# Kernel tuning notes

Measured on AMD Instinct MI355X. Metric: run time of the kernel, lower is better.

The kernel has to match this reference:

```python
import jax, jax.numpy as jnp
import numpy as np

INPUT_DIM, LATENT_DIM, HIDDEN_DIM, BATCH = 1024, 128, 1024, 32768


def setup_inputs() -> dict:
    key = jax.random.key(0)
    ks = jax.random.split(key, 12)
    s = 0.02
    x = (jax.random.uniform(ks[0], (BATCH, INPUT_DIM)) < 0.5).astype(jnp.float32)  # binary data
    eps = jax.random.normal(ks[1], (BATCH, LATENT_DIM), dtype=jnp.float32)
    return {
        "x": x,
        "eps": eps,
        "We1": jax.random.normal(ks[2], (INPUT_DIM, HIDDEN_DIM)) * s,
        "be1": jnp.zeros((HIDDEN_DIM,), jnp.float32),
        "Wmu": jax.random.normal(ks[3], (HIDDEN_DIM, LATENT_DIM)) * s,
        "bmu": jnp.zeros((LATENT_DIM,), jnp.float32),
        "Wls": jax.random.normal(ks[4], (HIDDEN_DIM, LATENT_DIM)) * s,
        "bls": jnp.zeros((LATENT_DIM,), jnp.float32),
        "Wd1": jax.random.normal(ks[5], (LATENT_DIM, HIDDEN_DIM)) * s,
        "bd1": jnp.zeros((HIDDEN_DIM,), jnp.float32),
        "Wd2": jax.random.normal(ks[6], (HIDDEN_DIM, INPUT_DIM)) * s,
        "bd2": jnp.zeros((INPUT_DIM,), jnp.float32),
    }


def reference(x, eps, We1, be1, Wmu, bmu, Wls, bls, Wd1, bd1, Wd2, bd2):
    # Encoder: one hidden ReLU layer, mu / logsigma heads
    h = jax.nn.relu(x @ We1 + be1)                      # [B, H]
    mu = h @ Wmu + bmu                                  # [B, L]
    logsigma = h @ Wls + bls                            # [B, L]
    # Reparameterization: z = sigma * eps + mu (vectorized diag(exp(logsigma)) @ eps)
    z = mu + jnp.exp(logsigma) * eps                    # [B, L]
    # Decoder: one hidden ReLU layer, sigmoid Bernoulli params
    hd = jax.nn.relu(z @ Wd1 + bd1)                     # [B, H]
    theta = jax.nn.sigmoid(hd @ Wd2 + bd2)              # [B, D]
    # Bernoulli log-likelihood: sum_j log(theta^x * (1-theta)^(1-x))
    log_px = jnp.sum(x * jnp.log(theta) + (1.0 - x) * jnp.log1p(-theta), axis=-1)  # [B]
    # KL(q||N(0,I)) = 0.5 * sum(sigma^2 + mu^2 - log(sigma^2) - 1)
    kl = 0.5 * jnp.sum(jnp.exp(2.0 * logsigma) + mu * mu - 2.0 * logsigma - 1.0, axis=-1)  # [B]
    return log_px - kl                                  # elbo_mc [B]
```

## Files before the change

### kernel.cpp

```cpp
#include <hip/hip_runtime.h>
#include <cstdint>
#include <cstddef>


typedef __bf16 bf16x8 __attribute__((ext_vector_type(8)));
typedef float f32x4 __attribute__((ext_vector_type(4)));

__device__ __forceinline__ unsigned short f32_to_bf16(float f) {
  unsigned int u = __float_as_uint(f);
  u += 0x7fffu + ((u >> 16) & 1u);
  return (unsigned short)(u >> 16);
}

struct TransJob { const float* in; unsigned short* out; int K, N, blkEnd; };

__global__ void prep_k(TransJob j0, TransJob j1, TransJob j2,
                       TransJob j3, TransJob j4,
                       const float* __restrict__ x,
                       unsigned short* __restrict__ xbit,
                       int n4, int castBlocks) {
  __shared__ float tile[32][33];
  int bid = blockIdx.x;
  int tx = threadIdx.x, ty = threadIdx.y;
  if (bid >= j4.blkEnd) {
    int tid = ty * 32 + tx;
    int stride = castBlocks * 256;
    for (int i = (bid - j4.blkEnd) * 256 + tid; i < n4; i += stride) {
      float4 v = reinterpret_cast<const float4*>(x)[i];
      unsigned int nib = (v.x != 0.f ? 1u : 0u) | (v.y != 0.f ? 2u : 0u) |
                         (v.z != 0.f ? 4u : 0u) | (v.w != 0.f ? 8u : 0u);
      unsigned int n1 = __shfl_down(nib, 1, 64);
      unsigned int n2 = __shfl_down(nib, 2, 64);
      unsigned int n3 = __shfl_down(nib, 3, 64);
      if ((tid & 3) == 0)
        xbit[i >> 2] = (unsigned short)(nib | (n1 << 4) | (n2 << 8) | (n3 << 12));
    }
    return;
  }
  TransJob j; int base;
  if (bid < j0.blkEnd)      { j = j0; base = 0; }
  else if (bid < j1.blkEnd) { j = j1; base = j0.blkEnd; }
  else if (bid < j2.blkEnd) { j = j2; base = j1.blkEnd; }
  else if (bid < j3.blkEnd) { j = j3; base = j2.blkEnd; }
  else                      { j = j4; base = j3.blkEnd; }
  int local = bid - base;
  int gxN = j.N >> 5;
  int n0 = (local % gxN) * 32, k0 = (local / gxN) * 32;
#pragma unroll
  for (int r = 0; r < 32; r += 8)
    tile[ty + r][tx] = j.in[(size_t)(k0 + ty + r) * j.N + n0 + tx];
  __syncthreads();
#pragma unroll
  for (int r = 0; r < 32; r += 8)
    j.out[(size_t)(n0 + ty + r) * j.K + k0 + tx] = f32_to_bf16(tile[tx][ty + r]);
}

__device__ __forceinline__ void gl_lds16(const unsigned short* g, unsigned short* l) {
  __builtin_amdgcn_global_load_lds(
      (__attribute__((address_space(1))) void*)g,
      (__attribute__((address_space(3))) void*)l, 16, 0, 0);
}

template <int EPI, int TAG, int ABIT>
__global__ __launch_bounds__(512, 2) void gemm256(
    const unsigned short* __restrict__ A, const unsigned short* __restrict__ BT,
    int gx, int N, int K,
    const float* __restrict__ bias0,
    unsigned short* __restrict__ outb, float* __restrict__ outf,
    const unsigned short* __restrict__ xbit) {
  __shared__ __align__(16) unsigned short smem[65536];

  const int tid = threadIdx.x;
  const int lane = tid & 63;
  const int wave = tid >> 6;
  const int wr = wave >> 2;
  const int wc = wave & 3;
  const int lm = lane & 15, lq = lane >> 4;
  const int sw = lm & 7;

  const int bid = blockIdx.x;
  const int xcd = bid & 7;
  const int t8 = bid >> 3;
  const int m0 = (xcd + 8 * (t8 / gx)) * 256;
  const int n0 = (t8 % gx) * 256;
  const int NT = K >> 6;

  unsigned short* const smemp = smem;
  auto Abuf = [&](int b) -> unsigned short* {
    return ABIT ? smemp : smemp + b * 32768;
  };
  auto Bbuf = [&](int b) -> unsigned short* {
    return ABIT ? smemp + 16384 + b * 16384 : smemp + b * 32768 + 16384;
  };

  const unsigned short* gpA[2];
  const unsigned short* gpB[2];
  int loA[2], loB[2], xaddr[2];
#pragma unroll
  for (int r = 0; r < 2; ++r) {
    int c = tid + 512 * r, rl = c >> 3, q8 = c & 7;
    int rowA = (rl & 63) + ((rl >> 6) << 7);
    int rowB = (rl & 31) + ((rl >> 5) << 6);
    int qgA = q8 ^ (rowA & 7);
    gpA[r] = A + (size_t)(m0 + rowA) * K + qgA * 8;
    gpB[r] = BT + (size_t)(n0 + rowB) * K + (q8 ^ (rowB & 7)) * 8;
    loA[r] = rowA * 64 + q8 * 8;
    loB[r] = rowB * 64 + q8 * 8;
    xaddr[r] = rowA * 128 + qgA;
  }

  auto stage = [&](int kind, int buf, int kt) {
#pragma unroll
    for (int r = 0; r < 2; ++r) {
      if (kind == 0)      { if (!ABIT) gl_lds16(gpA[r] + kt * 64,          Abuf(buf) + loA[r]); }
      else if (kind == 3) { if (!ABIT) gl_lds16(gpA[r] + 64 * K + kt * 64, Abuf(buf) + loA[r] + 4096); }
      else if (kind == 1) gl_lds16(gpB[r] + kt * 64,          Bbuf(buf) + loB[r]);
      else                gl_lds16(gpB[r] + 32 * K + kt * 64, Bbuf(buf) + loB[r] + 2048);
    }
  };

  auto expandA = [&](int t) {
    const unsigned char* xsb = reinterpret_cast<const unsigned char*>(smemp + 49152);
    unsigned short* As = smemp;
#pragma unroll
    for (int r = 0; r < 2; ++r) {
#pragma unroll
      for (int h = 0; h < 2; ++h) {
        unsigned int b = xsb[xaddr[r] + h * 8192 + 8 * t];
        unsigned int o0 = ((b & 1u)        ? 0x3F80u : 0u) | ((b & 2u)   ? 0x3F800000u : 0u);
        unsigned int o1 = (((b >> 2) & 1u) ? 0x3F80u : 0u) | ((b & 8u)   ? 0x3F800000u : 0u);
        unsigned int o2 = (((b >> 4) & 1u) ? 0x3F80u : 0u) | ((b & 32u)  ? 0x3F800000u : 0u);
        unsigned int o3 = (((b >> 6) & 1u) ? 0x3F80u : 0u) | ((b & 128u) ? 0x3F800000u : 0u);
        *reinterpret_cast<uint4*>(As + loA[r] + h * 4096) = make_uint4(o0, o1, o2, o3);
      }
    }
  };

  if (ABIT) {
    const unsigned short* xp = xbit + (size_t)m0 * 64;
    unsigned short* xs = smemp + 49152;
#pragma unroll
    for (int i = 0; i < 4; ++i)
      gl_lds16(xp + (tid + 512 * i) * 8, xs + (tid + 512 * i) * 8);
    stage(1, 0, 0); stage(2, 0, 0);
    stage(1, 1, 1); stage(2, 1, 1);
    asm volatile("s_waitcnt vmcnt(8)" ::: "memory");
    expandA(0);
    asm volatile("s_waitcnt vmcnt(4) lgkmcnt(0)" ::: "memory");
    __builtin_amdgcn_s_barrier();
  } else {
    stage(0, 0, 0); stage(1, 0, 0); stage(2, 0, 0); stage(3, 0, 0);
    stage(0, 1, 1); stage(1, 1, 1); stage(2, 1, 1);
    asm volatile("s_waitcnt vmcnt(6)" ::: "memory");
    __builtin_amdgcn_s_barrier();
  }

  f32x4 acc[8][4] = {};

  const int aRow = (wr * 128 + lm) * 64;
  const int bRow = (wc * 64 + lm) * 64;
  const int c0 = ((0 | lq) ^ sw) * 8;
  const int c1 = ((4 | lq) ^ sw) * 8;

  for (int t = 0; t < NT; ++t) {
    const int b = t & 1;
    const unsigned short* Ab = Abuf(b);
    const unsigned short* Bb = Bbuf(b);
    bf16x8 af[4][2], bf1[2][2], bf2[2][2];

#pragma unroll
    for (int i = 0; i < 4; ++i) {
      af[i][0] = *reinterpret_cast<const bf16x8*>(Ab + aRow + i * 1024 + c0);
      af[i][1] = *reinterpret_cast<const bf16x8*>(Ab + aRow + i * 1024 + c1);
    }
#pragma unroll
    for (int j = 0; j < 2; ++j) {
      bf1[j][0] = *reinterpret_cast<const bf16x8*>(Bb + bRow + j * 1024 + c0);
      bf1[j][1] = *reinterpret_cast<const bf16x8*>(Bb + bRow + j * 1024 + c1);
    }
    if (!ABIT && t + 1 < NT) stage(3, (t + 1) & 1, t + 1);
    __builtin_amdgcn_s_barrier();
    asm volatile("s_waitcnt lgkmcnt(0)" ::: "memory");
    __builtin_amdgcn_sched_barrier(0);
    __builtin_amdgcn_s_setprio(1);
#pragma unroll
    for (int s = 0; s < 2; ++s)
#pragma unroll
      for (int i = 0; i < 4; ++i)
#pragma unroll
        for (int j = 0; j < 2; ++j)
          acc[i][j] = __builtin_amdgcn_mfma_f32_16x16x32_bf16(af[i][s], bf1[j][s], acc[i][j], 0, 0, 0);
    __builtin_amdgcn_s_setprio(0);
    __builtin_amdgcn_s_barrier();

#pragma unroll
    for (int j = 0; j < 2; ++j) {
      bf2[j][0] = *reinterpret_cast<const bf16x8*>(Bb + bRow + (j + 2) * 1024 + c0);
      bf2[j][1] = *reinterpret_cast<const bf16x8*>(Bb + bRow + (j + 2) * 1024 + c1);
    }
    if (t + 2 < NT) stage(ABIT ? 1 : 0, b, t + 2);
    __builtin_amdgcn_s_barrier();
    asm volatile("s_waitcnt lgkmcnt(0)" ::: "memory");
    __builtin_amdgcn_sched_barrier(0);
    __builtin_amdgcn_s_setprio(1);
#pragma unroll
    for (int s = 0; s < 2; ++s)
#pragma unroll
      for (int i = 0; i < 4; ++i)
#pragma unroll
        for (int j = 0; j < 2; ++j)
          acc[i][j + 2] = __builtin_amdgcn_mfma_f32_16x16x32_bf16(af[i][s], bf2[j][s], acc[i][j + 2], 0, 0, 0);
    __builtin_amdgcn_s_setprio(0);
    __builtin_amdgcn_s_barrier();

#pragma unroll
    for (int i = 0; i < 4; ++i) {
      af[i][0] = *reinterpret_cast<const bf16x8*>(Ab + aRow + (64 + i * 16) * 64 + c0);
      af[i][1] = *reinterpret_cast<const bf16x8*>(Ab + aRow + (64 + i * 16) * 64 + c1);
    }
    if (t + 2 < NT) stage(ABIT ? 2 : 1, b, t + 2);
    __builtin_amdgcn_s_barrier();
    asm volatile("s_waitcnt lgkmcnt(0)" ::: "memory");
    __builtin_amdgcn_sched_barrier(0);
    __builtin_amdgcn_s_setprio(1);
#pragma unroll
    for (int s = 0; s < 2; ++s)
#pragma unroll
      for (int i = 0; i < 4; ++i)
#pragma unroll
        for (int j = 0; j < 2; ++j)
          acc[i + 4][j] = __builtin_amdgcn_mfma_f32_16x16x32_bf16(af[i][s], bf1[j][s], acc[i + 4][j], 0, 0, 0);
    __builtin_amdgcn_s_setprio(0);
    __builtin_amdgcn_s_barrier();

    if (ABIT) { if (t + 1 < NT) expandA(t + 1); }
    else      { if (t + 2 < NT) stage(2, b, t + 2); }
    __builtin_amdgcn_s_barrier();
    __builtin_amdgcn_s_setprio(1);
#pragma unroll
    for (int s = 0; s < 2; ++s)
#pragma unroll
      for (int i = 0; i < 4; ++i)
#pragma unroll
        for (int j = 0; j < 2; ++j)
          acc[i + 4][j + 2] = __builtin_amdgcn_mfma_f32_16x16x32_bf16(af[i][s], bf2[j][s], acc[i + 4][j + 2], 0, 0, 0);
    __builtin_amdgcn_s_setprio(0);
    if (ABIT) {
      if (t + 2 < NT) { asm volatile("s_waitcnt vmcnt(4) lgkmcnt(0)" ::: "memory"); }
      else            { asm volatile("s_waitcnt vmcnt(0) lgkmcnt(0)" ::: "memory"); }
    } else {
      if (t + 2 < NT)      { asm volatile("s_waitcnt vmcnt(6)" ::: "memory"); }
      else if (t + 1 < NT) { asm volatile("s_waitcnt vmcnt(0)" ::: "memory"); }
    }
    __builtin_amdgcn_s_barrier();
  }

  if (EPI == 0) {
#pragma unroll
    for (int i = 0; i < 8; ++i)
#pragma unroll
      for (int j = 0; j < 4; ++j) {
        int col = n0 + wc * 64 + j * 16 + lm;
        float bias = bias0[col];
#pragma unroll
        for (int r = 0; r < 4; ++r) {
          int row = m0 + wr * 128 + i * 16 + lq * 4 + r;
          float v = acc[i][j][r] + bias;
          outb[(size_t)row * N + col] = f32_to_bf16(fmaxf(v, 0.f));
        }
      }
  } else {
    const int wpr = N >> 4;
#pragma unroll
    for (int i = 0; i < 8; ++i) {
      float rs[4] = {0.f, 0.f, 0.f, 0.f};
#pragma unroll
      for (int j = 0; j < 4; ++j) {
        int col = n0 + wc * 64 + j * 16 + lm;
        float bias = bias0[col];
        int w16 = (col >> 4);
#pragma unroll
        for (int r = 0; r < 4; ++r) {
          int row = m0 + wr * 128 + i * 16 + lq * 4 + r;
          float l = acc[i][j][r] + bias;
          unsigned short mask = xbit[(size_t)row * wpr + w16];
          float tt = ((mask >> lm) & 1) ? -l : l;
          float sp = fmaxf(tt, 0.f) + __logf(1.f + __expf(-fabsf(tt)));
          rs[r] -= sp;
        }
      }
#pragma unroll
      for (int off = 1; off < 16; off <<= 1)
#pragma unroll
        for (int r = 0; r < 4; ++r) rs[r] += __shfl_xor(rs[r], off, 64);
      if (lm == 0) {
#pragma unroll
        for (int r = 0; r < 4; ++r)
          atomicAdd(&outf[m0 + wr * 128 + i * 16 + lq * 4 + r], rs[r]);
      }
    }
  }
}

__global__ __launch_bounds__(256, 2) void latent_fused(
    const unsigned short* A,
    const unsigned short* __restrict__ BT,
    const unsigned short* __restrict__ WD1,
    const float* __restrict__ bmu, const float* __restrict__ bls,
    const float* __restrict__ bd1,
    const float* __restrict__ eps,
    unsigned short* hd,
    float* __restrict__ out) {
  __shared__ __align__(16) unsigned short smem[28672];
  unsigned short* As0 = smem;
  unsigned short* As1 = smem + 2048;
  unsigned short* Bs0 = smem + 4096;
  unsigned short* Bs1 = smem + 12288;
  unsigned short* zs  = smem + 20480;
  unsigned short* Bs2 = smem;

  const int K = 1024;
  const int tid = threadIdx.x;
  const int lane = tid & 63;
  const int wave = tid >> 6;
  const int m0 = blockIdx.x * 64;
  const int lm = lane & 15, lq = lane >> 4;
  const int sw2 = (lm >> 1) & 3;

  const unsigned short* agp;
  const unsigned short* bgp[4];
  {
    int row = tid >> 2, q = tid & 3;
    agp = A + (size_t)(m0 + row) * K + (q ^ ((row >> 1) & 3)) * 8;
  }
#pragma unroll
  for (int r = 0; r < 4; ++r) {
    int c = tid + 256 * r;
    int row = c >> 2, q = c & 3;
    bgp[r] = BT + (size_t)row * K + (q ^ ((row >> 1) & 3)) * 8;
  }

  auto stage1 = [&](int buf, int kt) {
    gl_lds16(agp + kt, (buf ? As1 : As0) + tid * 8);
    unsigned short* Bd = buf ? Bs1 : Bs0;
#pragma unroll
    for (int r = 0; r < 4; ++r) gl_lds16(bgp[r] + kt, Bd + (tid + 256 * r) * 8);
  };

  f32x4 acc[16] = {};

  stage1(0, 0);
  __syncthreads();

  const int aOff = (wave * 16 + lm) * 32 + (lq ^ sw2) * 8;
  for (int t = 0; t < 32; ++t) {
    const int cur = t & 1;
    if (t + 1 < 32) stage1(cur ^ 1, (t + 1) * 32);
    const unsigned short* Ab = cur ? As1 : As0;
    const unsigned short* Bb = cur ? Bs1 : Bs0;
    bf16x8 af = *reinterpret_cast<const bf16x8*>(Ab + aOff);
#pragma unroll
    for (int j = 0; j < 16; ++j) {
      bf16x8 b = *reinterpret_cast<const bf16x8*>(Bb + (j * 16 + lm) * 32 + (lq ^ sw2) * 8);
      acc[j] = __builtin_amdgcn_mfma_f32_16x16x32_bf16(af, b, acc[j], 0, 0, 0);
    }
    __syncthreads();
  }

  auto stage2 = [&](int hh) {
#pragma unroll
    for (int ri = 0; ri < 8; ++ri) {
      int c = tid + 256 * ri;
      int row = c >> 4, slot = c & 15;
      int gc = slot ^ (row & 7);
      gl_lds16(WD1 + (size_t)(hh * 128 + row) * 128 + gc * 8, Bs2 + c * 8);
    }
  };
  stage2(0);

  {
    float kl[4] = {0.f, 0.f, 0.f, 0.f};
#pragma unroll
    for (int j = 0; j < 8; ++j) {
      int dim = j * 16 + lm;
      float bm = bmu[dim], bl = bls[dim];
#pragma unroll
      for (int r = 0; r < 4; ++r) {
        int rowl = wave * 16 + lq * 4 + r;
        float mu = acc[j][r] + bm;
        float ls = acc[j + 8][r] + bl;
        float e = eps[(size_t)(m0 + rowl) * 128 + dim];
        float zv = fmaf(__expf(ls), e, mu);
        int chunk = (dim >> 3);
        int slot = chunk ^ (rowl & 7);
        zs[rowl * 128 + slot * 8 + (lm & 7)] = f32_to_bf16(zv);
        kl[r] += 0.5f * (__expf(2.f * ls) + mu * mu - 2.f * ls - 1.f);
      }
    }
#pragma unroll
    for (int off = 1; off < 16; off <<= 1)
#pragma unroll
      for (int r = 0; r < 4; ++r) kl[r] += __shfl_xor(kl[r], off, 64);
    if (lm == 0) {
#pragma unroll
      for (int r = 0; r < 4; ++r)
        out[m0 + wave * 16 + lq * 4 + r] = -kl[r];
    }
  }

  for (int hh = 0; hh < 8; ++hh) {
    asm volatile("s_waitcnt vmcnt(0)" ::: "memory");
    __syncthreads();
    f32x4 acc2[8] = {};
#pragma unroll
    for (int ks = 0; ks < 4; ++ks) {
      const int cks = (ks * 4 + lq) ^ (lm & 7);
      bf16x8 a0 = *reinterpret_cast<const bf16x8*>(zs + (wave * 16 + lm) * 128 + cks * 8);
#pragma unroll
      for (int j = 0; j < 8; ++j) {
        bf16x8 b = *reinterpret_cast<const bf16x8*>(Bs2 + (j * 16 + lm) * 128 + cks * 8);
        acc2[j] = __builtin_amdgcn_mfma_f32_16x16x32_bf16(a0, b, acc2[j], 0, 0, 0);
      }
    }
    __syncthreads();
    if (hh + 1 < 8) stage2(hh + 1);
#pragma unroll
    for (int j = 0; j < 8; ++j) {
      int col = hh * 128 + j * 16 + lm;
      float bias = bd1[col];
#pragma unroll
      for (int r = 0; r < 4; ++r) {
        int row = m0 + wave * 16 + lq * 4 + r;
        float v = acc2[j][r] + bias;
        hd[(size_t)row * 1024 + col] = f32_to_bf16(fmaxf(v, 0.f));
      }
    }
  }
}

extern "C" void kernel_launch(void* const* d_in, const int* in_sizes, int n_in,
                              void* d_out, int out_size, void* d_ws, size_t ws_size,
                              hipStream_t stream) {
  const float* x   = (const float*)d_in[0];
  const float* eps = (const float*)d_in[1];
  const float* We1 = (const float*)d_in[2];
  const float* be1 = (const float*)d_in[3];
  const float* Wmu = (const float*)d_in[4];
  const float* bmu = (const float*)d_in[5];
  const float* Wls = (const float*)d_in[6];
  const float* bls = (const float*)d_in[7];
  const float* Wd1 = (const float*)d_in[8];
  const float* bd1 = (const float*)d_in[9];
  const float* Wd2 = (const float*)d_in[10];
  const float* bd2 = (const float*)d_in[11];
  float* out = (float*)d_out;

  const int B = 32768, D = 1024, H = 1024, L = 128;

  char* ws = (char*)d_ws;
  size_t off = 0;
  auto alloc = [&](size_t bytes) {
    void* p = ws + off;
    off += (bytes + 255) & ~(size_t)255;
    return p;
  };
  unsigned short* xbit = (unsigned short*)alloc((size_t)B * D / 8);
  unsigned short* w1t  = (unsigned short*)alloc((size_t)H * D * 2);
  unsigned short* w2t  = (unsigned short*)alloc((size_t)256 * H * 2);
  unsigned short* wd1t = (unsigned short*)alloc((size_t)H * L * 2);
  unsigned short* wd2t = (unsigned short*)alloc((size_t)D * H * 2);
  unsigned short* h    = (unsigned short*)alloc((size_t)B * H * 2);
  unsigned short* hd   = h;

  TransJob j0{We1, w1t, D, H, 1024};
  TransJob j1{Wmu, w2t, H, L, 1152};
  TransJob j2{Wls, w2t + 128 * H, H, L, 1280};
  TransJob j3{Wd1, wd1t, L, H, 1408};
  TransJob j4{Wd2, wd2t, H, D, 2432};
  prep_k<<<2432 + 2048, dim3(32, 8), 0, stream>>>(
      j0, j1, j2, j3, j4, x, xbit, B * D / 4, 2048);

  gemm256<0, 1, 1><<<512, 512, 0, stream>>>(
      nullptr, w1t, 4, H, D, be1, h, nullptr, xbit);
  latent_fused<<<B / 64, 256, 0, stream>>>(
      h, w2t, wd1t, bmu, bls, bd1, eps, hd, out);
  gemm256<2, 4, 0><<<512, 512, 0, stream>>>(
      hd, wd2t, 4, D, H, bd2, nullptr, out, xbit);

  (void)in_sizes; (void)n_in; (void)out_size; (void)ws_size;
}
```

Baseline: 430.2 us.

## Loop two N tiles per block in first GEMM, split decoder GEMM, double-buffer Wd1

The first GEMM now launches 256 blocks, and each block loops over two 256-column N tiles, reusing the bit-packed x row block already loaded into LDS. The decoder output GEMM is split into two launches covering the two halves of the M dimension. The latent kernel's Wd1 staging becomes double-buffered 64-row chunks, so the next chunk is prefetched while the current one computes instead of sitting behind a full sync. The goal is to cut redundant x loads and hide weight-load latency, at the cost of fewer blocks per launch and one extra kernel launch.

```diff
diff --git a/kernel.cpp b/kernel.cpp
--- a/kernel.cpp
+++ b/kernel.cpp
@@ -64,7 +64,7 @@
 template <int EPI, int TAG, int ABIT>
 __global__ __launch_bounds__(512, 2) void gemm256(
     const unsigned short* __restrict__ A, const unsigned short* __restrict__ BT,
-    int gx, int N, int K,
+    int mBase, int N, int K,
     const float* __restrict__ bias0,
     unsigned short* __restrict__ outb, float* __restrict__ outf,
     const unsigned short* __restrict__ xbit) {
@@ -81,8 +81,9 @@
   const int bid = blockIdx.x;
   const int xcd = bid & 7;
   const int t8 = bid >> 3;
-  const int m0 = (xcd + 8 * (t8 / gx)) * 256;
-  const int n0 = (t8 % gx) * 256;
+  int m0, n0base;
+  if (ABIT) { m0 = (xcd + 8 * (t8 >> 1)) * 256; n0base = (t8 & 1) * 512; }
+  else      { m0 = mBase + (xcd + 8 * (t8 >> 2)) * 256; n0base = (t8 & 3) * 256; }
   const int NT = K >> 6;
 
   unsigned short* const smemp = smem;
@@ -94,7 +95,7 @@
   };
 
   const unsigned short* gpA[2];
-  const unsigned short* gpB[2];
+  const unsigned short* gpB0[2];
   int loA[2], loB[2], xaddr[2];
 #pragma unroll
   for (int r = 0; r < 2; ++r) {
@@ -103,21 +104,11 @@
     int rowB = (rl & 31) + ((rl >> 5) << 6);
     int qgA = q8 ^ (rowA & 7);
     gpA[r] = A + (size_t)(m0 + rowA) * K + qgA * 8;
-    gpB[r] = BT + (size_t)(n0 + rowB) * K + (q8 ^ (rowB & 7)) * 8;
+    gpB0[r] = BT + (size_t)rowB * K + (q8 ^ (rowB & 7)) * 8;
     loA[r] = rowA * 64 + q8 * 8;
     loB[r] = rowB * 64 + q8 * 8;
     xaddr[r] = rowA * 128 + qgA;
   }
-
-  auto stage = [&](int kind, int buf, int kt) {
-#pragma unroll
-    for (int r = 0; r < 2; ++r) {
-      if (kind == 0)      { if (!ABIT) gl_lds16(gpA[r] + kt * 64,          Abuf(buf) + loA[r]); }
-      else if (kind == 3) { if (!ABIT) gl_lds16(gpA[r] + 64 * K + kt * 64, Abuf(buf) + loA[r] + 4096); }
-      else if (kind == 1) gl_lds16(gpB[r] + kt * 64,          Bbuf(buf) + loB[r]);
-      else                gl_lds16(gpB[r] + 32 * K + kt * 64, Bbuf(buf) + loB[r] + 2048);
-    }
-  };
 
   auto expandA = [&](int t) {
     const unsigned char* xsb = reinterpret_cast<const unsigned char*>(smemp + 49152);
@@ -136,167 +127,187 @@
     }
   };
 
-  if (ABIT) {
-    const unsigned short* xp = xbit + (size_t)m0 * 64;
-    unsigned short* xs = smemp + 49152;
-#pragma unroll
-    for (int i = 0; i < 4; ++i)
-      gl_lds16(xp + (tid + 512 * i) * 8, xs + (tid + 512 * i) * 8);
-    stage(1, 0, 0); stage(2, 0, 0);
-    stage(1, 1, 1); stage(2, 1, 1);
-    asm volatile("s_waitcnt vmcnt(8)" ::: "memory");
-    expandA(0);
-    asm volatile("s_waitcnt vmcnt(4) lgkmcnt(0)" ::: "memory");
-    __builtin_amdgcn_s_barrier();
-  } else {
-    stage(0, 0, 0); stage(1, 0, 0); stage(2, 0, 0); stage(3, 0, 0);
-    stage(0, 1, 1); stage(1, 1, 1); stage(2, 1, 1);
-    asm volatile("s_waitcnt vmcnt(6)" ::: "memory");
-    __builtin_amdgcn_s_barrier();
-  }
-
-  f32x4 acc[8][4] = {};
-
   const int aRow = (wr * 128 + lm) * 64;
   const int bRow = (wc * 64 + lm) * 64;
   const int c0 = ((0 | lq) ^ sw) * 8;
   const int c1 = ((4 | lq) ^ sw) * 8;
 
-  for (int t = 0; t < NT; ++t) {
-    const int b = t & 1;
-    const unsigned short* Ab = Abuf(b);
-    const unsigned short* Bb = Bbuf(b);
-    bf16x8 af[4][2], bf1[2][2], bf2[2][2];
-
-#pragma unroll
-    for (int i = 0; i < 4; ++i) {
-      af[i][0] = *reinterpret_cast<const bf16x8*>(Ab + aRow + i * 1024 + c0);
-      af[i][1] = *reinterpret_cast<const bf16x8*>(Ab + aRow + i * 1024 + c1);
-    }
-#pragma unroll
-    for (int j = 0; j < 2; ++j) {
-      bf1[j][0] = *reinterpret_cast<const bf16x8*>(Bb + bRow + j * 1024 + c0);
-      bf1[j][1] = *reinterpret_cast<const bf16x8*>(Bb + bRow + j * 1024 + c1);
-    }
-    if (!ABIT && t + 1 < NT) stage(3, (t + 1) & 1, t + 1);
-    __builtin_amdgcn_s_barrier();
-    asm volatile("s_waitcnt lgkmcnt(0)" ::: "memory");
-    __builtin_amdgcn_sched_barrier(0);
-    __builtin_amdgcn_s_setprio(1);
-#pragma unroll
-    for (int s = 0; s < 2; ++s)
-#pragma unroll
-      for (int i = 0; i < 4; ++i)
-#pragma unroll
-        for (int j = 0; j < 2; ++j)
-          acc[i][j] = __builtin_amdgcn_mfma_f32_16x16x32_bf16(af[i][s], bf1[j][s], acc[i][j], 0, 0, 0);
-    __builtin_amdgcn_s_setprio(0);
-    __builtin_amdgcn_s_barrier();
-
-#pragma unroll
-    for (int j = 0; j < 2; ++j) {
-      bf2[j][0] = *reinterpret_cast<const bf16x8*>(Bb + bRow + (j + 2) * 1024 + c0);
-      bf2[j][1] = *reinterpret_cast<const bf16x8*>(Bb + bRow + (j + 2) * 1024 + c1);
-    }
-    if (t + 2 < NT) stage(ABIT ? 1 : 0, b, t + 2);
-    __builtin_amdgcn_s_barrier();
-    asm volatile("s_waitcnt lgkmcnt(0)" ::: "memory");
-    __builtin_amdgcn_sched_barrier(0);
-    __builtin_amdgcn_s_setprio(1);
-#pragma unroll
-    for (int s = 0; s < 2; ++s)
-#pragma unroll
-      for (int i = 0; i < 4; ++i)
-#pragma unroll
-        for (int j = 0; j < 2; ++j)
-          acc[i][j + 2] = __builtin_amdgcn_mfma_f32_16x16x32_bf16(af[i][s], bf2[j][s], acc[i][j + 2], 0, 0, 0);
-    __builtin_amdgcn_s_setprio(0);
-    __builtin_amdgcn_s_barrier();
-
-#pragma unroll
-    for (int i = 0; i < 4; ++i) {
-      af[i][0] = *reinterpret_cast<const bf16x8*>(Ab + aRow + (64 + i * 16) * 64 + c0);
-      af[i][1] = *reinterpret_cast<const bf16x8*>(Ab + aRow + (64 + i * 16) * 64 + c1);
-    }
-    if (t + 2 < NT) stage(ABIT ? 2 : 1, b, t + 2);
-    __builtin_amdgcn_s_barrier();
-    asm volatile("s_waitcnt lgkmcnt(0)" ::: "memory");
-    __builtin_amdgcn_sched_barrier(0);
-    __builtin_amdgcn_s_setprio(1);
-#pragma unroll
-    for (int s = 0; s < 2; ++s)
-#pragma unroll
-      for (int i = 0; i < 4; ++i)
-#pragma unroll
-        for (int j = 0; j < 2; ++j)
-          acc[i + 4][j] = __builtin_amdgcn_mfma_f32_16x16x32_bf16(af[i][s], bf1[j][s], acc[i + 4][j], 0, 0, 0);
-    __builtin_amdgcn_s_setprio(0);
-    __builtin_amdgcn_s_barrier();
-
-    if (ABIT) { if (t + 1 < NT) expandA(t + 1); }
-    else      { if (t + 2 < NT) stage(2, b, t + 2); }
-    __builtin_amdgcn_s_barrier();
-    __builtin_amdgcn_s_setprio(1);
-#pragma unroll
-    for (int s = 0; s < 2; ++s)
-#pragma unroll
-      for (int i = 0; i < 4; ++i)
-#pragma unroll
-        for (int j = 0; j < 2; ++j)
-          acc[i + 4][j + 2] = __builtin_amdgcn_mfma_f32_16x16x32_bf16(af[i][s], bf2[j][s], acc[i + 4][j + 2], 0, 0, 0);
-    __builtin_amdgcn_s_setprio(0);
+  const int NTL = ABIT ? 2 : 1;
+  for (int ntl = 0; ntl < NTL; ++ntl) {
+    const int n0 = n0base + ntl * 256;
+    const unsigned short* gB[2];
+#pragma unroll
+    for (int r = 0; r < 2; ++r) gB[r] = gpB0[r] + (size_t)n0 * K;
+
+    auto stage = [&](int kind, int buf, int kt) {
+#pragma unroll
+      for (int r = 0; r < 2; ++r) {
+        if (kind == 0)      { if (!ABIT) gl_lds16(gpA[r] + kt * 64,          Abuf(buf) + loA[r]); }
+        else if (kind == 3) { if (!ABIT) gl_lds16(gpA[r] + 64 * K + kt * 64, Abuf(buf) + loA[r] + 4096); }
+        else if (kind == 1) gl_lds16(gB[r] + kt * 64,          Bbuf(buf) + loB[r]);
+        else                gl_lds16(gB[r] + 32 * K + kt * 64, Bbuf(buf) + loB[r] + 2048);
+      }
+    };
+
     if (ABIT) {
-      if (t + 2 < NT) { asm volatile("s_waitcnt vmcnt(4) lgkmcnt(0)" ::: "memory"); }
-      else            { asm volatile("s_waitcnt vmcnt(0) lgkmcnt(0)" ::: "memory"); }
+      if (ntl == 0) {
+        const unsigned short* xp = xbit + (size_t)m0 * 64;
+        unsigned short* xs = smemp + 49152;
+#pragma unroll
+        for (int i = 0; i < 4; ++i)
+          gl_lds16(xp + (tid + 512 * i) * 8, xs + (tid + 512 * i) * 8);
+      }
+      stage(1, 0, 0); stage(2, 0, 0);
+      stage(1, 1, 1); stage(2, 1, 1);
+      if (ntl == 0) { asm volatile("s_waitcnt vmcnt(8)" ::: "memory"); }
+      expandA(0);
+      asm volatile("s_waitcnt vmcnt(4) lgkmcnt(0)" ::: "memory");
+      __builtin_amdgcn_s_barrier();
     } else {
-      if (t + 2 < NT)      { asm volatile("s_waitcnt vmcnt(6)" ::: "memory"); }
-      else if (t + 1 < NT) { asm volatile("s_waitcnt vmcnt(0)" ::: "memory"); }
-    }
-    __builtin_amdgcn_s_barrier();
-  }
-
-  if (EPI == 0) {
-#pragma unroll
-    for (int i = 0; i < 8; ++i)
-#pragma unroll
-      for (int j = 0; j < 4; ++j) {
-        int col = n0 + wc * 64 + j * 16 + lm;
-        float bias = bias0[col];
-#pragma unroll
-        for (int r = 0; r < 4; ++r) {
-          int row = m0 + wr * 128 + i * 16 + lq * 4 + r;
-          float v = acc[i][j][r] + bias;
-          outb[(size_t)row * N + col] = f32_to_bf16(fmaxf(v, 0.f));
+      stage(0, 0, 0); stage(1, 0, 0); stage(2, 0, 0); stage(3, 0, 0);
+      stage(0, 1, 1); stage(1, 1, 1); stage(2, 1, 1);
+      asm volatile("s_waitcnt vmcnt(6)" ::: "memory");
+      __builtin_amdgcn_s_barrier();
+    }
+
+    f32x4 acc[8][4] = {};
+
+    for (int t = 0; t < NT; ++t) {
+      const int b = t & 1;
+      const unsigned short* Ab = Abuf(b);
+      const unsigned short* Bb = Bbuf(b);
+      bf16x8 af[4][2], bf1[2][2], bf2[2][2];
+
+#pragma unroll
+      for (int i = 0; i < 4; ++i) {
+        af[i][0] = *reinterpret_cast<const bf16x8*>(Ab + aRow + i * 1024 + c0);
+        af[i][1] = *reinterpret_cast<const bf16x8*>(Ab + aRow + i * 1024 + c1);
+      }
+#pragma unroll
+      for (int j = 0; j < 2; ++j) {
+        bf1[j][0] = *reinterpret_cast<const bf16x8*>(Bb + bRow + j * 1024 + c0);
+        bf1[j][1] = *reinterpret_cast<const bf16x8*>(Bb + bRow + j * 1024 + c1);
+      }
+      if (!ABIT && t + 1 < NT) stage(3, (t + 1) & 1, t + 1);
+      __builtin_amdgcn_s_barrier();
+      asm volatile("s_waitcnt lgkmcnt(0)" ::: "memory");
+      __builtin_amdgcn_sched_barrier(0);
+      __builtin_amdgcn_s_setprio(1);
+#pragma unroll
+      for (int s = 0; s < 2; ++s)
+#pragma unroll
+        for (int i = 0; i < 4; ++i)
+#pragma unroll
+          for (int j = 0; j < 2; ++j)
+            acc[i][j] = __builtin_amdgcn_mfma_f32_16x16x32_bf16(af[i][s], bf1[j][s], acc[i][j], 0, 0, 0);
+      __builtin_amdgcn_s_setprio(0);
+      __builtin_amdgcn_s_barrier();
+
+#pragma unroll
+      for (int j = 0; j < 2; ++j) {
+        bf2[j][0] = *reinterpret_cast<const bf16x8*>(Bb + bRow + (j + 2) * 1024 + c0);
+        bf2[j][1] = *reinterpret_cast<const bf16x8*>(Bb + bRow + (j + 2) * 1024 + c1);
+      }
+      if (t + 2 < NT) stage(ABIT ? 1 : 0, b, t + 2);
+      __builtin_amdgcn_s_barrier();
+      asm volatile("s_waitcnt lgkmcnt(0)" ::: "memory");
+      __builtin_amdgcn_sched_barrier(0);
+      __builtin_amdgcn_s_setprio(1);
+#pragma unroll
+      for (int s = 0; s < 2; ++s)
+#pragma unroll
+        for (int i = 0; i < 4; ++i)
+#pragma unroll
+          for (int j = 0; j < 2; ++j)
+            acc[i][j + 2] = __builtin_amdgcn_mfma_f32_16x16x32_bf16(af[i][s], bf2[j][s], acc[i][j + 2], 0, 0, 0);
+      __builtin_amdgcn_s_setprio(0);
+      __builtin_amdgcn_s_barrier();
+
+#pragma unroll
+      for (int i = 0; i < 4; ++i) {
+        af[i][0] = *reinterpret_cast<const bf16x8*>(Ab + aRow + (64 + i * 16) * 64 + c0);
+        af[i][1] = *reinterpret_cast<const bf16x8*>(Ab + aRow + (64 + i * 16) * 64 + c1);
+      }
+      if (t + 2 < NT) stage(ABIT ? 2 : 1, b, t + 2);
+      __builtin_amdgcn_s_barrier();
+      asm volatile("s_waitcnt lgkmcnt(0)" ::: "memory");
+      __builtin_amdgcn_sched_barrier(0);
+      __builtin_amdgcn_s_setprio(1);
+#pragma unroll
+      for (int s = 0; s < 2; ++s)
+#pragma unroll
+        for (int i = 0; i < 4; ++i)
+#pragma unroll
+          for (int j = 0; j < 2; ++j)
+            acc[i + 4][j] = __builtin_amdgcn_mfma_f32_16x16x32_bf16(af[i][s], bf1[j][s], acc[i + 4][j], 0, 0, 0);
+      __builtin_amdgcn_s_setprio(0);
+      __builtin_amdgcn_s_barrier();
+
+      if (ABIT) { if (t + 1 < NT) expandA(t + 1); }
+      else      { if (t + 2 < NT) stage(2, b, t + 2); }
+      __builtin_amdgcn_s_barrier();
+      __builtin_amdgcn_s_setprio(1);
+#pragma unroll
+      for (int s = 0; s < 2; ++s)
+#pragma unroll
+        for (int i = 0; i < 4; ++i)
+#pragma unroll
+          for (int j = 0; j < 2; ++j)
+            acc[i + 4][j + 2] = __builtin_amdgcn_mfma_f32_16x16x32_bf16(af[i][s], bf2[j][s], acc[i + 4][j + 2], 0, 0, 0);
+      __builtin_amdgcn_s_setprio(0);
+      if (ABIT) {
+        if (t + 2 < NT) { asm volatile("s_waitcnt vmcnt(4) lgkmcnt(0)" ::: "memory"); }
+        else            { asm volatile("s_waitcnt vmcnt(0) lgkmcnt(0)" ::: "memory"); }
+      } else {
+        if (t + 2 < NT)      { asm volatile("s_waitcnt vmcnt(6)" ::: "memory"); }
+        else if (t + 1 < NT) { asm volatile("s_waitcnt vmcnt(0)" ::: "memory"); }
+      }
+      __builtin_amdgcn_s_barrier();
+    }
+
+    if (EPI == 0) {
+#pragma unroll
+      for (int i = 0; i < 8; ++i)
+#pragma unroll
+        for (int j = 0; j < 4; ++j) {
+          int col = n0 + wc * 64 + j * 16 + lm;
+          float bias = bias0[col];
+#pragma unroll
+          for (int r = 0; r < 4; ++r) {
+            int row = m0 + wr * 128 + i * 16 + lq * 4 + r;
+            float v = acc[i][j][r] + bias;
+            outb[(size_t)row * N + col] = f32_to_bf16(fmaxf(v, 0.f));
+          }
         }
-      }
-  } else {
-    const int wpr = N >> 4;
-#pragma unroll
-    for (int i = 0; i < 8; ++i) {
-      float rs[4] = {0.f, 0.f, 0.f, 0.f};
-#pragma unroll
-      for (int j = 0; j < 4; ++j) {
-        int col = n0 + wc * 64 + j * 16 + lm;
-        float bias = bias0[col];
-        int w16 = (col >> 4);
-#pragma unroll
-        for (int r = 0; r < 4; ++r) {
-          int row = m0 + wr * 128 + i * 16 + lq * 4 + r;
-          float l = acc[i][j][r] + bias;
-          unsigned short mask = xbit[(size_t)row * wpr + w16];
-          float tt = ((mask >> lm) & 1) ? -l : l;
-          float sp = fmaxf(tt, 0.f) + __logf(1.f + __expf(-fabsf(tt)));
-          rs[r] -= sp;
+    } else {
+      const int wpr = N >> 4;
+#pragma unroll
+      for (int i = 0; i < 8; ++i) {
+        float rs[4] = {0.f, 0.f, 0.f, 0.f};
+#pragma unroll
+        for (int j = 0; j < 4; ++j) {
+          int col = n0 + wc * 64 + j * 16 + lm;
+          float bias = bias0[col];
+          int w16 = (col >> 4);
+#pragma unroll
+          for (int r = 0; r < 4; ++r) {
+            int row = m0 + wr * 128 + i * 16 + lq * 4 + r;
+            float l = acc[i][j][r] + bias;
+            unsigned short mask = xbit[(size_t)row * wpr + w16];
+            float tt = ((mask >> lm) & 1) ? -l : l;
+            float sp = fmaxf(tt, 0.f) + __logf(1.f + __expf(-fabsf(tt)));
+            rs[r] -= sp;
+          }
         }
-      }
-#pragma unroll
-      for (int off = 1; off < 16; off <<= 1)
-#pragma unroll
-        for (int r = 0; r < 4; ++r) rs[r] += __shfl_xor(rs[r], off, 64);
-      if (lm == 0) {
-#pragma unroll
-        for (int r = 0; r < 4; ++r)
-          atomicAdd(&outf[m0 + wr * 128 + i * 16 + lq * 4 + r], rs[r]);
+#pragma unroll
+        for (int off = 1; off < 16; off <<= 1)
+#pragma unroll
+          for (int r = 0; r < 4; ++r) rs[r] += __shfl_xor(rs[r], off, 64);
+        if (lm == 0) {
+#pragma unroll
+          for (int r = 0; r < 4; ++r)
+            atomicAdd(&outf[m0 + wr * 128 + i * 16 + lq * 4 + r], rs[r]);
+        }
       }
     }
   }
@@ -317,7 +328,8 @@
   unsigned short* Bs0 = smem + 4096;
   unsigned short* Bs1 = smem + 12288;
   unsigned short* zs  = smem + 20480;
-  unsigned short* Bs2 = smem;
+  unsigned short* Bq0 = smem;
+  unsigned short* Bq1 = smem + 8192;
 
   const int K = 1024;
   const int tid = threadIdx.x;
@@ -367,16 +379,17 @@
     __syncthreads();
   }
 
-  auto stage2 = [&](int hh) {
-#pragma unroll
-    for (int ri = 0; ri < 8; ++ri) {
+  auto stage2 = [&](int q, int buf) {
+    unsigned short* D = buf ? Bq1 : Bq0;
+#pragma unroll
+    for (int ri = 0; ri < 4; ++ri) {
       int c = tid + 256 * ri;
       int row = c >> 4, slot = c & 15;
       int gc = slot ^ (row & 7);
-      gl_lds16(WD1 + (size_t)(hh * 128 + row) * 128 + gc * 8, Bs2 + c * 8);
+      gl_lds16(WD1 + (size_t)(q * 64 + row) * 128 + gc * 8, D + c * 8);
     }
   };
-  stage2(0);
+  stage2(0, 0);
 
   {
     float kl[4] = {0.f, 0.f, 0.f, 0.f};
@@ -408,25 +421,26 @@
     }
   }
 
-  for (int hh = 0; hh < 8; ++hh) {
-    asm volatile("s_waitcnt vmcnt(0)" ::: "memory");
-    __syncthreads();
-    f32x4 acc2[8] = {};
+  for (int q = 0; q < 16; ++q) {
+    if (q == 0) { asm volatile("s_waitcnt vmcnt(0) lgkmcnt(0)" ::: "memory"); }
+    else        { asm volatile("s_waitcnt vmcnt(16)" ::: "memory"); }
+    __builtin_amdgcn_s_barrier();
+    if (q + 1 < 16) stage2(q + 1, (q + 1) & 1);
+    const unsigned short* Bq = (q & 1) ? Bq1 : Bq0;
+    f32x4 acc2[4] = {};
 #pragma unroll
     for (int ks = 0; ks < 4; ++ks) {
       const int cks = (ks * 4 + lq) ^ (lm & 7);
       bf16x8 a0 = *reinterpret_cast<const bf16x8*>(zs + (wave * 16 + lm) * 128 + cks * 8);
 #pragma unroll
-      for (int j = 0; j < 8; ++j) {
-        bf16x8 b = *reinterpret_cast<const bf16x8*>(Bs2 + (j * 16 + lm) * 128 + cks * 8);
+      for (int j = 0; j < 4; ++j) {
+        bf16x8 b = *reinterpret_cast<const bf16x8*>(Bq + (j * 16 + lm) * 128 + cks * 8);
         acc2[j] = __builtin_amdgcn_mfma_f32_16x16x32_bf16(a0, b, acc2[j], 0, 0, 0);
       }
     }
-    __syncthreads();
-    if (hh + 1 < 8) stage2(hh + 1);
-#pragma unroll
-    for (int j = 0; j < 8; ++j) {
-      int col = hh * 128 + j * 16 + lm;
+#pragma unroll
+    for (int j = 0; j < 4; ++j) {
+      int col = q * 64 + j * 16 + lm;
       float bias = bd1[col];
 #pragma unroll
       for (int r = 0; r < 4; ++r) {
@@ -480,12 +494,14 @@
   prep_k<<<2432 + 2048, dim3(32, 8), 0, stream>>>(
       j0, j1, j2, j3, j4, x, xbit, B * D / 4, 2048);
 
-  gemm256<0, 1, 1><<<512, 512, 0, stream>>>(
-      nullptr, w1t, 4, H, D, be1, h, nullptr, xbit);
+  gemm256<0, 1, 1><<<256, 512, 0, stream>>>(
+      nullptr, w1t, 0, H, D, be1, h, nullptr, xbit);
   latent_fused<<<B / 64, 256, 0, stream>>>(
       h, w2t, wd1t, bmu, bls, bd1, eps, hd, out);
-  gemm256<2, 4, 0><<<512, 512, 0, stream>>>(
-      hd, wd2t, 4, D, H, bd2, nullptr, out, xbit);
+  gemm256<2, 40, 0><<<256, 512, 0, stream>>>(
+      hd, wd2t, 0, D, H, bd2, nullptr, out, xbit);
+  gemm256<2, 41, 0><<<256, 512, 0, stream>>>(
+      hd, wd2t, 16384, D, H, bd2, nullptr, out, xbit);
 
   (void)in_sizes; (void)n_in; (void)out_size; (void)ws_size;
 }
```

Result: slower. 556.9 us (+29.5%).

## Re-tile latent encoder GEMM so each wave owns latent columns across all rows

Applied to the files above, without the earlier changes.

In the fused latent kernel's mu/logsigma GEMM, each wave previously computed 16 rows across all 256 output columns, reading 16 B fragments per A fragment. Now each wave computes all 64 rows for its own 32 mu and 32 logsigma columns, using a 4x4 fragment grid. This cuts LDS fragment reads per MFMA from 17 per 16 to 8 per 16. Because each wave now holds only a slice of latent dims, the per-row KL sum is reduced across waves through a small shared-memory buffer plus an extra barrier.

```diff
diff --git a/kernel.cpp b/kernel.cpp
--- a/kernel.cpp
+++ b/kernel.cpp
@@ -311,12 +311,13 @@
     const float* __restrict__ eps,
     unsigned short* hd,
     float* __restrict__ out) {
-  __shared__ __align__(16) unsigned short smem[28672];
+  __shared__ __align__(16) unsigned short smem[29184];
   unsigned short* As0 = smem;
   unsigned short* As1 = smem + 2048;
   unsigned short* Bs0 = smem + 4096;
   unsigned short* Bs1 = smem + 12288;
   unsigned short* zs  = smem + 20480;
+  float* klbuf = reinterpret_cast<float*>(smem + 28672);
   unsigned short* Bs2 = smem;
 
   const int K = 1024;
@@ -347,23 +348,31 @@
     for (int r = 0; r < 4; ++r) gl_lds16(bgp[r] + kt, Bd + (tid + 256 * r) * 8);
   };
 
-  f32x4 acc[16] = {};
+  f32x4 acc[4][4] = {};
 
   stage1(0, 0);
   __syncthreads();
 
-  const int aOff = (wave * 16 + lm) * 32 + (lq ^ sw2) * 8;
+  const int cOff = (lq ^ sw2) * 8;
   for (int t = 0; t < 32; ++t) {
     const int cur = t & 1;
     if (t + 1 < 32) stage1(cur ^ 1, (t + 1) * 32);
     const unsigned short* Ab = cur ? As1 : As0;
     const unsigned short* Bb = cur ? Bs1 : Bs0;
-    bf16x8 af = *reinterpret_cast<const bf16x8*>(Ab + aOff);
-#pragma unroll
-    for (int j = 0; j < 16; ++j) {
-      bf16x8 b = *reinterpret_cast<const bf16x8*>(Bb + (j * 16 + lm) * 32 + (lq ^ sw2) * 8);
-      acc[j] = __builtin_amdgcn_mfma_f32_16x16x32_bf16(af, b, acc[j], 0, 0, 0);
-    }
+    bf16x8 af[4], bfr[4];
+#pragma unroll
+    for (int i = 0; i < 4; ++i)
+      af[i] = *reinterpret_cast<const bf16x8*>(Ab + (i * 16 + lm) * 32 + cOff);
+#pragma unroll
+    for (int j = 0; j < 4; ++j) {
+      int jj = (j < 2) ? (2 * wave + j) : (8 + 2 * wave + (j - 2));
+      bfr[j] = *reinterpret_cast<const bf16x8*>(Bb + (jj * 16 + lm) * 32 + cOff);
+    }
+#pragma unroll
+    for (int i = 0; i < 4; ++i)
+#pragma unroll
+      for (int j = 0; j < 4; ++j)
+        acc[i][j] = __builtin_amdgcn_mfma_f32_16x16x32_bf16(af[i], bfr[j], acc[i][j], 0, 0, 0);
     __syncthreads();
   }
 
@@ -378,17 +387,18 @@
   };
   stage2(0);
 
-  {
+#pragma unroll
+  for (int i = 0; i < 4; ++i) {
     float kl[4] = {0.f, 0.f, 0.f, 0.f};
 #pragma unroll
-    for (int j = 0; j < 8; ++j) {
-      int dim = j * 16 + lm;
+    for (int j = 0; j < 2; ++j) {
+      int dim = (2 * wave + j) * 16 + lm;
       float bm = bmu[dim], bl = bls[dim];
 #pragma unroll
       for (int r = 0; r < 4; ++r) {
-        int rowl = wave * 16 + lq * 4 + r;
-        float mu = acc[j][r] + bm;
-        float ls = acc[j + 8][r] + bl;
+        int rowl = i * 16 + lq * 4 + r;
+        float mu = acc[i][j][r] + bm;
+        float ls = acc[i][j + 2][r] + bl;
         float e = eps[(size_t)(m0 + rowl) * 128 + dim];
         float zv = fmaf(__expf(ls), e, mu);
         int chunk = (dim >> 3);
@@ -404,8 +414,13 @@
     if (lm == 0) {
 #pragma unroll
       for (int r = 0; r < 4; ++r)
-        out[m0 + wave * 16 + lq * 4 + r] = -kl[r];
-    }
+        klbuf[wave * 64 + i * 16 + lq * 4 + r] = kl[r];
+    }
+  }
+  __syncthreads();
+  if (tid < 64) {
+    float s = klbuf[tid] + klbuf[64 + tid] + klbuf[128 + tid] + klbuf[192 + tid];
+    out[m0 + tid] = -s;
   }
 
   for (int hh = 0; hh < 8; ++hh) {
```

After: 429.4 us. No clear change (-0.2%).
